# Performance work log

Hardware: AMD Instinct MI355X
Metric: run time of the kernel (lower is better)

Reference implementation:

```python
import jax, jax.numpy as jnp
import numpy as np

GAMMA = 2
EPS = 1e-8


def setup_inputs() -> dict:
    key = jax.random.key(0)
    kx, kw = jax.random.split(key)
    B, C, D, W, H = 4, 256, 16, 16, 16
    x = jax.random.normal(kx, (B, C, D, W, H), dtype=jnp.float32)
    # Conv3d(chan, chan, kernel_size=1) == per-voxel linear: weight (C_out, C_in), bias (C_out,)
    Wt = jax.random.normal(kw, (C, C), dtype=jnp.float32) * 0.02
    b = jnp.zeros((C,), dtype=jnp.float32)
    return {"x": x, "W": Wt, "b": b}


def reference(x, W, b):
    B, C, D, Wd, H = x.shape
    N = D * Wd * H
    xf = x.reshape(B, C, N)                                  # b c n
    # torch cosine_similarity(dim=1): dot / max(|xi|*|xj|, eps)
    norm = jnp.linalg.norm(xf, axis=1, keepdims=True)        # b 1 n
    xn = xf / jnp.maximum(norm, EPS)
    sim = jnp.einsum('bcn,bcm->bnm', xn, xn)                 # b n n (cosine)
    sim = jax.nn.relu(sim) ** GAMMA
    # transform_net: 1x1x1 conv = channel-mixing GEMM per voxel
    t = jnp.einsum('oc,bcm->bom', W, xf) + b[None, :, None]  # b c m
    out = jnp.einsum('bnm,bcm->bcn', sim, t)                 # b c n
    return out.reshape(B, C, D, Wd, H)
```

## Files before the change

### kernel.cpp

```cpp
#include <hip/hip_runtime.h>
#include <hip/hip_bf16.h>


typedef unsigned short u16;
typedef __attribute__((ext_vector_type(8))) short short8;
typedef __attribute__((ext_vector_type(4))) float f32x4;

#define MFMA16(a, b, c) __builtin_amdgcn_mfma_f32_16x16x32_bf16((a), (b), (c), 0, 0, 0)

__device__ __forceinline__ u16 f2bf(float f) {
    union { float f; unsigned u; } v; v.f = f;
    unsigned u = v.u;
    u += 0x7fffu + ((u >> 16) & 1u);
    return (u16)(u >> 16);
}

__device__ __forceinline__ unsigned cvtpk(float lo, float hi) {
    unsigned r;
    asm("v_cvt_pk_bf16_f32 %0, %1, %2" : "=v"(r) : "v"(lo), "v"(hi));
    return r;
}

__global__ __launch_bounds__(256) void k_prep(const float* __restrict__ x,
                                              const float* __restrict__ W,
                                              u16* __restrict__ xff,
                                              u16* __restrict__ Wf,
                                              float* __restrict__ nrm) {
    __shared__ float xs[256][65];
    __shared__ float part[4][64];
    __shared__ float rs_s[64];
    int bid = blockIdx.x;
    int b = bid >> 6, nt = bid & 63, n0 = nt << 6;
    int tid = threadIdx.x;

    if (bid < 32) {
        int q = (bid << 8) + tid;
        int lane = q & 63, kc = (q >> 6) & 7, ci = (q >> 9) & 3, wq = q >> 11;
        int row = (wq << 6) + (ci << 4) + (lane & 15);
        int col = (kc << 5) + ((lane >> 4) << 3);
        const float* wp = W + row * 256 + col;
        u16 tmp[8];
#pragma unroll
        for (int j = 0; j < 8; ++j) tmp[j] = f2bf(wp[j]);
        *(short8*)(Wf + ((size_t)q << 3)) = *(const short8*)tmp;
    }

    int rowg = tid >> 4, l16 = tid & 15;
    const float* xb = x + ((size_t)b << 20) + n0;
#pragma unroll
    for (int s = 0; s < 16; ++s) {
        int row = (s << 4) + rowg;
        float4 v = *(const float4*)(xb + (size_t)row * 4096 + (l16 << 2));
        xs[row][(l16 << 2) + 0] = v.x;
        xs[row][(l16 << 2) + 1] = v.y;
        xs[row][(l16 << 2) + 2] = v.z;
        xs[row][(l16 << 2) + 3] = v.w;
    }
    __syncthreads();
    int q2 = tid >> 6, nl = tid & 63;
    float ss = 0.f;
#pragma unroll 16
    for (int c = 0; c < 64; ++c) {
        float v = xs[(q2 << 6) + c][nl];
        ss += v * v;
    }
    part[q2][nl] = ss;
    __syncthreads();
    if (tid < 64) {
        float t = part[0][tid] + part[1][tid] + part[2][tid] + part[3][tid];
        float nr = sqrtf(t);
        nrm[(b << 12) + n0 + tid] = nr;
        rs_s[tid] = 1.0f / fmaxf(nr, 1e-8f);
    }
    __syncthreads();

    u16* xo = xff + ((size_t)b << 20) + ((size_t)nt << 14);
    int lane = tid & 63;
#pragma unroll
    for (int s = 0; s < 8; ++s) {
        int w2 = (s << 2) + (tid >> 6);
        int tl = ((w2 & 3) << 4) + (tid & 15);
        int c8 = ((w2 >> 2) << 2) + ((tid >> 4) & 3);
        float rsv = rs_s[tl];
        u16 tmp[8];
#pragma unroll
        for (int j = 0; j < 8; ++j)
            tmp[j] = f2bf(xs[(c8 << 3) + j][tl] * rsv);
        int chunk = ((tl >> 4) << 3) + (c8 >> 2);
        *(short8*)(xo + (chunk << 9) + (lane << 3)) = *(const short8*)tmp;
    }
}

__global__ __launch_bounds__(256) void k_tgemm(const u16* __restrict__ Wf,
                                               const u16* __restrict__ xff,
                                               const float* __restrict__ bias,
                                               const float* __restrict__ nrm,
                                               u16* __restrict__ tbf) {
    __shared__ u16 lds_t[256][72];
    int bid = blockIdx.x;
    int b = bid >> 6, mt = bid & 63;
    const u16* xf_t = xff + ((size_t)b << 20) + ((size_t)mt << 14);
    int tid = threadIdx.x, wid = tid >> 6, lane = tid & 63, lg = lane >> 4, lr = lane & 15;

    f32x4 zero = {0.f, 0.f, 0.f, 0.f};
    f32x4 acc[4][4];
#pragma unroll
    for (int ci = 0; ci < 4; ++ci)
#pragma unroll
        for (int mj = 0; mj < 4; ++mj) acc[ci][mj] = zero;

#pragma unroll
    for (int kc = 0; kc < 8; ++kc) {
        short8 afr[4], bfr[4];
#pragma unroll
        for (int ci = 0; ci < 4; ++ci)
            afr[ci] = *(const short8*)(Wf + ((size_t)((((wid << 2) + ci) << 3) + kc) << 9)
                                       + (lane << 3));
#pragma unroll
        for (int mj = 0; mj < 4; ++mj)
            bfr[mj] = *(const short8*)(xf_t + ((size_t)(((mj << 3) + kc)) << 9)
                                       + (lane << 3));
#pragma unroll
        for (int ci = 0; ci < 4; ++ci)
#pragma unroll
            for (int mj = 0; mj < 4; ++mj)
                acc[ci][mj] = MFMA16(afr[ci], bfr[mj], acc[ci][mj]);
    }
    float nv[4];
#pragma unroll
    for (int mj = 0; mj < 4; ++mj)
        nv[mj] = nrm[(b << 12) + (mt << 6) + (mj << 4) + lr];
#pragma unroll
    for (int ci = 0; ci < 4; ++ci) {
#pragma unroll
        for (int r = 0; r < 4; ++r) {
            int c = (wid << 6) + (ci << 4) + (lg << 2) + r;
            float bv = bias[c];
#pragma unroll
            for (int mj = 0; mj < 4; ++mj)
                lds_t[c][(mj << 4) + lr] = f2bf(acc[ci][mj][r] * nv[mj] + bv);
        }
    }
    __syncthreads();
    u16* to = tbf + ((size_t)b << 20) + ((size_t)mt << 14);
#pragma unroll
    for (int s = 0; s < 8; ++s) {
        int w2 = (s << 2) + (tid >> 6);
        int cq = w2 >> 3, ci2 = (w2 >> 1) & 3, k2 = w2 & 1;
        short8 v = *(const short8*)(&lds_t[(cq << 6) + (ci2 << 4) + lr][(k2 << 5) + (lg << 3)]);
        *(short8*)(to + (w2 << 9) + (lane << 3)) = v;
    }
}

__global__ __launch_bounds__(512) void k_fused(const u16* __restrict__ xff,
                                               const u16* __restrict__ tbf,
                                               float* __restrict__ out) {
    __shared__ __align__(16) u16 lds_p[8][4096];

#define PBYTE(row, col) ((((row) << 7) + ((col) << 1)) ^ (((row) & 7) << 4))
#define BAR() do { asm volatile("s_waitcnt lgkmcnt(0)" ::: "memory");              \
    __builtin_amdgcn_sched_barrier(0); __builtin_amdgcn_s_barrier();               \
    __builtin_amdgcn_sched_barrier(0); } while (0)

    int bid = blockIdx.x;
    int xcd = bid & 7, grp = bid >> 3;
    int batch = xcd >> 1;
    int nt = grp + 32 * (xcd & 1);
    int n0 = nt << 6;

    const u16* xf_b = xff + ((size_t)batch << 20);
    const u16* tb_f = tbf + ((size_t)batch << 20);
    float* out_b = out + ((size_t)batch << 20);

    int tid = threadIdx.x;
    int wid = tid >> 6, lane = tid & 63, lg = lane >> 4, lr = lane & 15;
    int lane8 = lane << 3;
    f32x4 zero = {0.f, 0.f, 0.f, 0.f};
    char* pbase = (char*)&lds_p[0][0];

    if (wid < 4) {
        int tc = wid;
        int colw = (tc << 4) + lr;
        short8 afrag[4][8];
#pragma unroll
        for (int rt = 0; rt < 4; ++rt)
#pragma unroll
            for (int kc = 0; kc < 8; ++kc)
                afrag[rt][kc] = *(const short8*)(xf_b
                    + ((size_t)((((nt << 2) + rt) << 3) + kc) << 9) + lane8);
        const u16* bb = xf_b + ((size_t)(tc << 3) << 9);
        short8 bfrA[8], bfrB[8];

#define RLDB(BUF, OFF)                                                                     \
        { _Pragma("unroll")                                                                \
          for (int kc = 0; kc < 8; ++kc)                                                   \
              BUF[kc] = *(const short8*)(bb + (OFF) + (kc << 9) + lane8); }

#define SCOMP(BUF, SLOT)                                                                   \
    {                                                                                      \
        f32x4 sac[4];                                                                      \
        _Pragma("unroll") for (int c = 0; c < 4; ++c) sac[c] = zero;                       \
        __builtin_amdgcn_s_setprio(1);                                                     \
        _Pragma("unroll")                                                                  \
        for (int kc = 0; kc < 8; ++kc) {                                                   \
            sac[0] = MFMA16(afrag[0][kc], BUF[kc], sac[0]);                                \
            sac[1] = MFMA16(afrag[1][kc], BUF[kc], sac[1]);                                \
            sac[2] = MFMA16(afrag[2][kc], BUF[kc], sac[2]);                                \
            sac[3] = MFMA16(afrag[3][kc], BUF[kc], sac[3]);                                \
        }                                                                                  \
        __builtin_amdgcn_s_setprio(0);                                                     \
        char* pd = pbase + ((SLOT) << 13);                                                 \
        _Pragma("unroll")                                                                  \
        for (int c = 0; c < 4; ++c) {                                                      \
            float q0 = fmaxf(sac[c][0], 0.f); q0 *= q0;                                    \
            float q1 = fmaxf(sac[c][1], 0.f); q1 *= q1;                                    \
            float q2 = fmaxf(sac[c][2], 0.f); q2 *= q2;                                    \
            float q3 = fmaxf(sac[c][3], 0.f); q3 *= q3;                                    \
            unsigned d01 = cvtpk(q0, q1);                                                  \
            unsigned d23 = cvtpk(q2, q3);                                                  \
            int rw = (lg << 2) + (c << 4);                                                 \
            *(u16*)(pd + PBYTE(rw, colw)) = (u16)d01;                                      \
            *(u16*)(pd + PBYTE(rw + 1, colw)) = (u16)(d01 >> 16);                          \
            *(u16*)(pd + PBYTE(rw + 2, colw)) = (u16)d23;                                  \
            *(u16*)(pd + PBYTE(rw + 3, colw)) = (u16)(d23 >> 16);                          \
        }                                                                                  \
    }

#define PPH_FULL(S0, S1, S2, S3)                                                           \
        SCOMP(bfrA, S0); RLDB(bfrA, 2 * 16384);                                            \
        SCOMP(bfrB, S1); RLDB(bfrB, 3 * 16384);                                            \
        SCOMP(bfrA, S2); RLDB(bfrA, 4 * 16384);                                            \
        SCOMP(bfrB, S3); RLDB(bfrB, 5 * 16384);                                            \
        bb += 4 * 16384; BAR();

        RLDB(bfrA, 0);
        RLDB(bfrB, 16384);
        PPH_FULL(0, 1, 2, 3);
        for (int pp = 0; pp < 7; ++pp) {
            PPH_FULL(4, 5, 6, 7);
            PPH_FULL(0, 1, 2, 3);
        }
        SCOMP(bfrA, 4); RLDB(bfrA, 2 * 16384);
        SCOMP(bfrB, 5); RLDB(bfrB, 3 * 16384);
        SCOMP(bfrA, 6);
        SCOMP(bfrB, 7);
        BAR();
        BAR();
#undef PPH_FULL
#undef SCOMP
#undef RLDB
    } else {
        int cq = wid - 4;
        const u16* tbse = tb_f + ((size_t)(cq << 3) << 9);
        short8 tbcA[4][2], tbcB[4][2];

#define RLDT(TB, OFF)                                                                      \
        { _Pragma("unroll")                                                                \
          for (int ci = 0; ci < 4; ++ci) {                                                 \
              _Pragma("unroll")                                                            \
              for (int k2 = 0; k2 < 2; ++k2)                                               \
                  TB[ci][k2] = *(const short8*)(tbse + (OFF)                               \
                                                + ((((ci << 1) + k2)) << 9) + lane8); } }

#define RDP(PFR, SLOT)                                                                     \
    {                                                                                      \
        char* pc = pbase + ((SLOT) << 13);                                                 \
        _Pragma("unroll")                                                                  \
        for (int nj = 0; nj < 4; ++nj) {                                                   \
            PFR[nj][0] = *(const short8*)(pc + PBYTE((nj << 4) + lr, (lg << 3)));          \
            PFR[nj][1] = *(const short8*)(pc + PBYTE((nj << 4) + lr, 32 + (lg << 3)));     \
        }                                                                                  \
    }

#define OMMA(TC, PFR)                                                                      \
    {                                                                                      \
        __builtin_amdgcn_s_setprio(1);                                                     \
        _Pragma("unroll")                                                                  \
        for (int ci = 0; ci < 4; ++ci) {                                                   \
            _Pragma("unroll")                                                              \
            for (int nj = 0; nj < 4; ++nj) {                                               \
                oacc[ci][nj] = MFMA16(TC[ci][0], PFR[nj][0], oacc[ci][nj]);                \
                oacc[ci][nj] = MFMA16(TC[ci][1], PFR[nj][1], oacc[ci][nj]);                \
            }                                                                              \
        }                                                                                  \
        __builtin_amdgcn_s_setprio(0);                                                     \
    }

#define CPH(S0, S1, S2, S3, MODE)                                                          \
    {                                                                                      \
        short8 pfA[4][2], pfB[4][2];                                                       \
        RDP(pfA, S0); RDP(pfB, S1);                                                        \
        OMMA(tbcA, pfA);                                                                   \
        if ((MODE) >= 1) RLDT(tbcA, 2 * 16384);                                            \
        RDP(pfA, S2);                                                                      \
        OMMA(tbcB, pfB);                                                                   \
        if ((MODE) >= 1) RLDT(tbcB, 3 * 16384);                                            \
        RDP(pfB, S3);                                                                      \
        OMMA(tbcA, pfA);                                                                   \
        if ((MODE) >= 2) RLDT(tbcA, 4 * 16384);                                            \
        OMMA(tbcB, pfB);                                                                   \
        if ((MODE) >= 2) RLDT(tbcB, 5 * 16384);                                            \
        if ((MODE) >= 2) tbse += 4 * 16384;                                                \
        BAR();                                                                             \
    }

        RLDT(tbcA, 0);
        RLDT(tbcB, 16384);
        f32x4 oacc[4][4];
#pragma unroll
        for (int ci = 0; ci < 4; ++ci)
#pragma unroll
            for (int nj = 0; nj < 4; ++nj) oacc[ci][nj] = zero;
        BAR();

        for (int pp = 0; pp < 7; ++pp) {
            CPH(0, 1, 2, 3, 2);
            CPH(4, 5, 6, 7, 2);
        }
        CPH(0, 1, 2, 3, 2);
        CPH(4, 5, 6, 7, 1);
#undef CPH
#undef OMMA
#undef RDP
#undef RLDT

#pragma unroll
        for (int ci = 0; ci < 4; ++ci) {
            int c = (cq << 6) + (ci << 4) + (lg << 2);
#pragma unroll
            for (int nj = 0; nj < 4; ++nj) {
                int n = n0 + (nj << 4) + lr;
                float* op = out_b + (size_t)c * 4096 + n;
#pragma unroll
                for (int r = 0; r < 4; ++r) op[(size_t)r * 4096] = oacc[ci][nj][r];
            }
        }
    }
#undef PBYTE
#undef BAR
}

extern "C" void kernel_launch(void* const* d_in, const int* in_sizes, int n_in,
                              void* d_out, int out_size, void* d_ws, size_t ws_size,
                              hipStream_t stream) {
    const float* x = (const float*)d_in[0];
    const float* W = (const float*)d_in[1];
    const float* bias = (const float*)d_in[2];
    float* out = (float*)d_out;

    char* ws = (char*)d_ws;
    u16* xff = (u16*)ws;
    u16* tbf = (u16*)(ws + ((size_t)8 << 20));
    u16* Wf = (u16*)(ws + ((size_t)16 << 20));
    float* nrm = (float*)(ws + ((size_t)16 << 20) + (192u << 10));

    hipLaunchKernelGGL(k_prep, dim3(256), dim3(256), 0, stream, x, W, xff, Wf, nrm);
    hipLaunchKernelGGL(k_tgemm, dim3(256), dim3(256), 0, stream, Wf, xff, bias, nrm, tbf);
    hipLaunchKernelGGL(k_fused, dim3(256), dim3(512), 0, stream, xff, tbf, out);
}
```

Measured before the change: 76.43 us.

## Deepen producer/consumer pipeline with triple-buffered T fragments and finer barriers

Reworks the warp-specialized schedule in the fused kernel. Producer waves now hit a barrier after every two P slots instead of every four. Consumer waves rotate three register buffers of transform-GEMM fragments, which lets global loads of T be issued one tile further ahead. The aim is to shorten the distance between producer and consumer stages and to hide global load latency better. The cost is more barriers per tile and higher register pressure in the consumer waves.

```diff
diff --git a/kernel.cpp b/kernel.cpp
--- a/kernel.cpp
+++ b/kernel.cpp
@@ -161,6 +161,7 @@
 #define BAR() do { asm volatile("s_waitcnt lgkmcnt(0)" ::: "memory");              \
     __builtin_amdgcn_sched_barrier(0); __builtin_amdgcn_s_barrier();               \
     __builtin_amdgcn_sched_barrier(0); } while (0)
+#define TS 16384
 
     int bid = blockIdx.x;
     int xcd = bid & 7, grp = bid >> 3;
@@ -226,33 +227,35 @@
         }                                                                                  \
     }
 
-#define PPH_FULL(S0, S1, S2, S3)                                                           \
-        SCOMP(bfrA, S0); RLDB(bfrA, 2 * 16384);                                            \
-        SCOMP(bfrB, S1); RLDB(bfrB, 3 * 16384);                                            \
-        SCOMP(bfrA, S2); RLDB(bfrA, 4 * 16384);                                            \
-        SCOMP(bfrB, S3); RLDB(bfrB, 5 * 16384);                                            \
-        bb += 4 * 16384; BAR();
-
         RLDB(bfrA, 0);
-        RLDB(bfrB, 16384);
-        PPH_FULL(0, 1, 2, 3);
-        for (int pp = 0; pp < 7; ++pp) {
-            PPH_FULL(4, 5, 6, 7);
-            PPH_FULL(0, 1, 2, 3);
-        }
-        SCOMP(bfrA, 4); RLDB(bfrA, 2 * 16384);
-        SCOMP(bfrB, 5); RLDB(bfrB, 3 * 16384);
+        RLDB(bfrB, TS);
+        SCOMP(bfrA, 0); RLDB(bfrA, 2 * TS);
+        SCOMP(bfrB, 1); RLDB(bfrB, 3 * TS);
+        BAR();
+        for (int g7 = 0; g7 < 7; ++g7) {
+            SCOMP(bfrA, 2); RLDB(bfrA, 4 * TS);
+            SCOMP(bfrB, 3); RLDB(bfrB, 5 * TS);  BAR();
+            SCOMP(bfrA, 4); RLDB(bfrA, 6 * TS);
+            SCOMP(bfrB, 5); RLDB(bfrB, 7 * TS);  BAR();
+            SCOMP(bfrA, 6); RLDB(bfrA, 8 * TS);
+            SCOMP(bfrB, 7); RLDB(bfrB, 9 * TS);  BAR();
+            SCOMP(bfrA, 0); RLDB(bfrA, 10 * TS);
+            SCOMP(bfrB, 1); RLDB(bfrB, 11 * TS); BAR();
+            bb += 8 * TS;
+        }
+        SCOMP(bfrA, 2); RLDB(bfrA, 4 * TS);
+        SCOMP(bfrB, 3); RLDB(bfrB, 5 * TS);  BAR();
+        SCOMP(bfrA, 4); RLDB(bfrA, 6 * TS);
+        SCOMP(bfrB, 5); RLDB(bfrB, 7 * TS);  BAR();
         SCOMP(bfrA, 6);
-        SCOMP(bfrB, 7);
+        SCOMP(bfrB, 7);  BAR();
         BAR();
-        BAR();
-#undef PPH_FULL
 #undef SCOMP
 #undef RLDB
     } else {
         int cq = wid - 4;
         const u16* tbse = tb_f + ((size_t)(cq << 3) << 9);
-        short8 tbcA[4][2], tbcB[4][2];
+        short8 tbcA[4][2], tbcB[4][2], tbcC[4][2];
 
 #define RLDT(TB, OFF)                                                                      \
         { _Pragma("unroll")                                                                \
@@ -286,26 +289,27 @@
         __builtin_amdgcn_s_setprio(0);                                                     \
     }
 
-#define CPH(S0, S1, S2, S3, MODE)                                                          \
+#define CGRP(s0, s1, s2, s3, s4, s5)                                                       \
     {                                                                                      \
         short8 pfA[4][2], pfB[4][2];                                                       \
-        RDP(pfA, S0); RDP(pfB, S1);                                                        \
-        OMMA(tbcA, pfA);                                                                   \
-        if ((MODE) >= 1) RLDT(tbcA, 2 * 16384);                                            \
-        RDP(pfA, S2);                                                                      \
-        OMMA(tbcB, pfB);                                                                   \
-        if ((MODE) >= 1) RLDT(tbcB, 3 * 16384);                                            \
-        RDP(pfB, S3);                                                                      \
-        OMMA(tbcA, pfA);                                                                   \
-        if ((MODE) >= 2) RLDT(tbcA, 4 * 16384);                                            \
-        OMMA(tbcB, pfB);                                                                   \
-        if ((MODE) >= 2) RLDT(tbcB, 5 * 16384);                                            \
-        if ((MODE) >= 2) tbse += 4 * 16384;                                                \
+        RDP(pfA, s0); RDP(pfB, s1);                                                        \
+        OMMA(tbcA, pfA); RLDT(tbcA, 3 * TS);                                               \
+        OMMA(tbcB, pfB); RLDT(tbcB, 4 * TS);                                               \
         BAR();                                                                             \
+        RDP(pfA, s2); RDP(pfB, s3);                                                        \
+        OMMA(tbcC, pfA); RLDT(tbcC, 5 * TS);                                               \
+        OMMA(tbcA, pfB); RLDT(tbcA, 6 * TS);                                               \
+        BAR();                                                                             \
+        RDP(pfA, s4); RDP(pfB, s5);                                                        \
+        OMMA(tbcB, pfA); RLDT(tbcB, 7 * TS);                                               \
+        OMMA(tbcC, pfB); RLDT(tbcC, 8 * TS);                                               \
+        BAR();                                                                             \
+        tbse += 6 * TS;                                                                    \
     }
 
         RLDT(tbcA, 0);
-        RLDT(tbcB, 16384);
+        RLDT(tbcB, TS);
+        RLDT(tbcC, 2 * TS);
         f32x4 oacc[4][4];
 #pragma unroll
         for (int ci = 0; ci < 4; ++ci)
@@ -313,13 +317,26 @@
             for (int nj = 0; nj < 4; ++nj) oacc[ci][nj] = zero;
         BAR();
 
-        for (int pp = 0; pp < 7; ++pp) {
-            CPH(0, 1, 2, 3, 2);
-            CPH(4, 5, 6, 7, 2);
-        }
-        CPH(0, 1, 2, 3, 2);
-        CPH(4, 5, 6, 7, 1);
-#undef CPH
+        for (int pp = 0; pp < 2; ++pp) {
+            CGRP(0, 1, 2, 3, 4, 5);
+            CGRP(6, 7, 0, 1, 2, 3);
+            CGRP(4, 5, 6, 7, 0, 1);
+            CGRP(2, 3, 4, 5, 6, 7);
+        }
+        CGRP(0, 1, 2, 3, 4, 5);
+        CGRP(6, 7, 0, 1, 2, 3);
+        {
+            short8 pfA[4][2], pfB[4][2];
+            RDP(pfA, 4); RDP(pfB, 5);
+            OMMA(tbcA, pfA); RLDT(tbcA, 3 * TS);
+            OMMA(tbcB, pfB);
+            BAR();
+            RDP(pfA, 6); RDP(pfB, 7);
+            OMMA(tbcC, pfA);
+            OMMA(tbcA, pfB);
+            BAR();
+        }
+#undef CGRP
 #undef OMMA
 #undef RDP
 #undef RLDT
@@ -338,6 +355,7 @@
     }
 #undef PBYTE
 #undef BAR
+#undef TS
 }
 
 extern "C" void kernel_launch(void* const* d_in, const int* in_sizes, int n_in,
```

After: 77.88 us. Within noise of the previous version (+1.9%).
